# Performance work log

Hardware: AMD Instinct MI355X
Metric: run time of the kernel (lower is better)

Reference implementation:

```python
import jax, jax.numpy as jnp
import numpy as np

SEQ = 4096
E = 2048

def setup_inputs() -> dict:
    key = jax.random.key(0)
    kx, kq, kk, kv = jax.random.split(key, 4)
    scale = 1.0 / np.sqrt(E)
    x = jax.random.normal(kx, (SEQ, E), dtype=jnp.float32)
    # nn.Linear weights: shape [out, in], applied as x @ W.T
    Wq = jax.random.uniform(kq, (E, E), dtype=jnp.float32, minval=-scale, maxval=scale)
    Wk = jax.random.uniform(kk, (E, E), dtype=jnp.float32, minval=-scale, maxval=scale)
    Wv = jax.random.uniform(kv, (E, E), dtype=jnp.float32, minval=-scale, maxval=scale)
    return {"x": x, "Wq": Wq, "Wk": Wk, "Wv": Wv}

def reference(x, Wq, Wk, Wv):
    # q/k/v projections: nn.Linear(bias=False) -> x @ W.T
    q = x @ Wq.T  # [S, E]
    k = x @ Wk.T  # [S, E]
    v = x @ Wv.T  # [S, E]
    s = q @ k.T  # [S, S]
    w = jax.nn.softmax(s / jnp.sqrt(jnp.float32(E)), axis=-1)
    return w @ v  # [S, E]
```

## Files before the change

kernel.cpp:

```cpp
#include <hip/hip_runtime.h>
#include <hip/hip_bf16.h>

#define S_DIM 4096
#define E_DIM 2048

typedef __attribute__((ext_vector_type(4))) float f32x4;
typedef __attribute__((ext_vector_type(8))) short bf16x8;

__device__ __forceinline__ unsigned short f2bf(float f) {
  unsigned u = __builtin_bit_cast(unsigned, f);
  u += 0x7FFFu + ((u >> 16) & 1u);
  return (unsigned short)(u >> 16);
}
__device__ __forceinline__ float bf2f(unsigned short h) {
  return __builtin_bit_cast(float, ((unsigned)h) << 16);
}

__global__ __launch_bounds__(256) void cast_kernel(const float* __restrict__ in,
                                                   unsigned short* __restrict__ out,
                                                   int n4) {
  int i = blockIdx.x * 256 + threadIdx.x;
  if (i >= n4) return;
  float4 v = reinterpret_cast<const float4*>(in)[i];
  ushort4 o;
  o.x = f2bf(v.x); o.y = f2bf(v.y); o.z = f2bf(v.z); o.w = f2bf(v.w);
  reinterpret_cast<ushort4*>(out)[i] = o;
}


__device__ __forceinline__ void stage_tile(char* lds_tile, const unsigned short* g,
                                           int row0, int k0, int ld, int tid) {
#pragma unroll
  for (int p = 0; p < 2; ++p) {
    const int off = tid * 16 + p * 4096;
    const int row = off >> 6;
    const int colb = off & 63;
    const char* ga = reinterpret_cast<const char*>(g + (size_t)(row0 + row) * ld + k0) + colb;
    char* la = lds_tile + (off & ~1023);
    __builtin_amdgcn_global_load_lds(
        (const __attribute__((address_space(1))) void*)ga,
        (__attribute__((address_space(3))) void*)la,
        16, 0, 0);
  }
}

enum { EPI_TBF16 = 1, EPI_F32 = 2, EPI_BF16 = 3 };

template <int EPI>
__global__ __launch_bounds__(256, 2) void gemm_nt(
    const unsigned short* __restrict__ A, const unsigned short* __restrict__ B,
    int lda, int ldb, int K,
    float* __restrict__ Cf, unsigned short* __restrict__ Cb,
    int ldc, float scale) {
  extern __shared__ char smem[];
  char* sA = smem;
  char* sB = smem + 8192;

  const int tid = threadIdx.x;
  const int row0A = blockIdx.y * 128;
  const int row0B = blockIdx.x * 128;

  const int wave = tid >> 6;
  const int lane = tid & 63;
  const int wr = (wave >> 1) * 64;
  const int wc = (wave & 1) * 64;
  const int l15 = lane & 15;
  const int kg = lane >> 4;

  f32x4 acc[4][4];
#pragma unroll
  for (int m = 0; m < 4; ++m)
#pragma unroll
    for (int n = 0; n < 4; ++n) acc[m][n] = (f32x4){0.f, 0.f, 0.f, 0.f};

  for (int kt = 0; kt < K; kt += 32) {
    __syncthreads();
    stage_tile(sA, A, row0A, kt, lda, tid);
    stage_tile(sB, B, row0B, kt, ldb, tid);
    __syncthreads();

    bf16x8 a_f[4], b_f[4];
#pragma unroll
    for (int m = 0; m < 4; ++m) {
      const int ra = (wr + m * 16 + l15) * 64 + kg * 16;
      const int rb = (wc + m * 16 + l15) * 64 + kg * 16;
      a_f[m] = *reinterpret_cast<const bf16x8*>(sA + ra);
      b_f[m] = *reinterpret_cast<const bf16x8*>(sB + rb);
    }
#pragma unroll
    for (int m = 0; m < 4; ++m)
#pragma unroll
      for (int n = 0; n < 4; ++n)
        acc[m][n] = __builtin_amdgcn_mfma_f32_16x16x32_bf16(a_f[m], b_f[n], acc[m][n], 0, 0, 0);
  }

#pragma unroll
  for (int m = 0; m < 4; ++m)
#pragma unroll
    for (int n = 0; n < 4; ++n) {
      const int row = row0A + wr + m * 16 + kg * 4;
      const int col = row0B + wc + n * 16 + l15;
      f32x4 v = acc[m][n];
      if constexpr (EPI == EPI_F32) {
#pragma unroll
        for (int r = 0; r < 4; ++r)
          Cf[(size_t)(row + r) * ldc + col] = v[r] * scale;
      } else if constexpr (EPI == EPI_BF16) {
#pragma unroll
        for (int r = 0; r < 4; ++r)
          Cb[(size_t)(row + r) * ldc + col] = f2bf(v[r] * scale);
      } else {
        unsigned short tmp[4];
#pragma unroll
        for (int r = 0; r < 4; ++r) tmp[r] = f2bf(v[r] * scale);
        ushort4 pk;
        pk.x = tmp[0]; pk.y = tmp[1]; pk.z = tmp[2]; pk.w = tmp[3];
        *reinterpret_cast<ushort4*>(Cb + (size_t)col * ldc + row) = pk;
      }
    }
}

__global__ __launch_bounds__(256) void softmax_kernel(const unsigned short* __restrict__ Sm,
                                                      unsigned short* __restrict__ P) {
  const int row = blockIdx.x;
  const int tid = threadIdx.x;
  const unsigned short* src = Sm + (size_t)row * S_DIM;
  float vals[16];
  float mx = -1e30f;
#pragma unroll
  for (int i = 0; i < 4; ++i) {
    ushort4 h = reinterpret_cast<const ushort4*>(src)[tid + i * 256];
    float a = bf2f(h.x), b = bf2f(h.y), c = bf2f(h.z), d = bf2f(h.w);
    vals[i * 4 + 0] = a; vals[i * 4 + 1] = b;
    vals[i * 4 + 2] = c; vals[i * 4 + 3] = d;
    mx = fmaxf(mx, fmaxf(fmaxf(a, b), fmaxf(c, d)));
  }
#pragma unroll
  for (int off = 32; off >= 1; off >>= 1) mx = fmaxf(mx, __shfl_xor(mx, off, 64));
  __shared__ float red[8];
  const int wave = tid >> 6, lane = tid & 63;
  if (lane == 0) red[wave] = mx;
  __syncthreads();
  mx = fmaxf(fmaxf(red[0], red[1]), fmaxf(red[2], red[3]));
  float sum = 0.f;
#pragma unroll
  for (int i = 0; i < 16; ++i) { vals[i] = __expf(vals[i] - mx); sum += vals[i]; }
#pragma unroll
  for (int off = 32; off >= 1; off >>= 1) sum += __shfl_xor(sum, off, 64);
  if (lane == 0) red[4 + wave] = sum;
  __syncthreads();
  sum = red[4] + red[5] + red[6] + red[7];
  const float inv = 1.0f / sum;
  unsigned short* dst = P + (size_t)row * S_DIM;
#pragma unroll
  for (int i = 0; i < 4; ++i) {
    ushort4 pk;
    pk.x = f2bf(vals[i * 4 + 0] * inv);
    pk.y = f2bf(vals[i * 4 + 1] * inv);
    pk.z = f2bf(vals[i * 4 + 2] * inv);
    pk.w = f2bf(vals[i * 4 + 3] * inv);
    reinterpret_cast<ushort4*>(dst)[tid + i * 256] = pk;
  }
}

extern "C" void kernel_launch(void* const* d_in, const int* in_sizes, int n_in,
                              void* d_out, int out_size, void* d_ws, size_t ws_size,
                              hipStream_t stream) {
  const float* x  = (const float*)d_in[0];
  const float* Wq = (const float*)d_in[1];
  const float* Wk = (const float*)d_in[2];
  const float* Wv = (const float*)d_in[3];
  float* out = (float*)d_out;
  char* ws = (char*)d_ws;

  const size_t MB = 1024 * 1024;
  const size_t NEED = 104 * MB;
  if (ws_size < NEED) return;

  unsigned short* qb = (unsigned short*)(ws);
  unsigned short* kb = (unsigned short*)(ws + 16 * MB);
  unsigned short* vt = (unsigned short*)(ws + 32 * MB);
  unsigned short* xb = (unsigned short*)(ws + 48 * MB);
  unsigned short* wb = (unsigned short*)(ws + 64 * MB);
  unsigned short* Sb = (unsigned short*)(ws + 72 * MB);
  unsigned short* P  = qb;

  const int nx4 = S_DIM * E_DIM / 4;
  const int nw4 = E_DIM * E_DIM / 4;

  cast_kernel<<<(nx4 + 255) / 256, 256, 0, stream>>>(x, xb, nx4);

  dim3 gProj(E_DIM / 128, S_DIM / 128);
  cast_kernel<<<(nw4 + 255) / 256, 256, 0, stream>>>(Wq, wb, nw4);
  gemm_nt<EPI_BF16><<<gProj, 256, 16384, stream>>>(
      xb, wb, E_DIM, E_DIM, E_DIM, nullptr, qb, E_DIM, 1.0f);
  cast_kernel<<<(nw4 + 255) / 256, 256, 0, stream>>>(Wk, wb, nw4);
  gemm_nt<EPI_BF16><<<gProj, 256, 16384, stream>>>(
      xb, wb, E_DIM, E_DIM, E_DIM, nullptr, kb, E_DIM, 1.0f);
  cast_kernel<<<(nw4 + 255) / 256, 256, 0, stream>>>(Wv, wb, nw4);
  gemm_nt<EPI_TBF16><<<gProj, 256, 16384, stream>>>(
      xb, wb, E_DIM, E_DIM, E_DIM, nullptr, vt, S_DIM, 1.0f);

  dim3 gQK(S_DIM / 128, S_DIM / 128);
  const float scale = 0.022097086912079608f;
  gemm_nt<EPI_BF16><<<gQK, 256, 16384, stream>>>(
      qb, kb, E_DIM, E_DIM, E_DIM, nullptr, Sb, S_DIM, scale);

  softmax_kernel<<<S_DIM, 256, 0, stream>>>(Sb, P);

  dim3 gPV(E_DIM / 128, S_DIM / 128);
  gemm_nt<EPI_F32><<<gPV, 256, 16384, stream>>>(
      P, vt, S_DIM, S_DIM, S_DIM, out, nullptr, E_DIM, 1.0f);
}
```

Measured before the change: 445.6 us.

## Replace GEMMs with 256x256 double-buffered 8-wave kernel, fuse QKV, split-K PV

Replaces the 128x128 single-buffered GEMM with a 512-thread kernel using 256x256 tiles and a 64-wide K step. It double-buffers LDS with swizzled async global-to-LDS loads and interleaves MFMA phases with barriers and priority hints. The three projections are fused into one GEMM over concatenated weights, and the P@V GEMM uses split-K over two partial buffers followed by an add kernel. This aims to raise MFMA utilisation and data reuse, at the cost of 128KB LDS per block, more workspace, and an extra reduction pass.

```diff
diff --git a/kernel.cpp b/kernel.cpp
--- a/kernel.cpp
+++ b/kernel.cpp
@@ -27,97 +27,205 @@
   reinterpret_cast<ushort4*>(out)[i] = o;
 }
 
-
-__device__ __forceinline__ void stage_tile(char* lds_tile, const unsigned short* g,
-                                           int row0, int k0, int ld, int tid) {
+__global__ __launch_bounds__(256) void add_kernel(const float* __restrict__ a,
+                                                  const float* __restrict__ b,
+                                                  float* __restrict__ o, int n4) {
+  int i = blockIdx.x * 256 + threadIdx.x;
+  if (i >= n4) return;
+  float4 va = reinterpret_cast<const float4*>(a)[i];
+  float4 vb = reinterpret_cast<const float4*>(b)[i];
+  float4 vo = {va.x + vb.x, va.y + vb.y, va.z + vb.z, va.w + vb.w};
+  reinterpret_cast<float4*>(o)[i] = vo;
+}
+
+
+__device__ __forceinline__ void stage_half(const unsigned short* __restrict__ g,
+                                           int grow0, int ld, int kByte0,
+                                           char* ldsHalfBase, int tid) {
 #pragma unroll
   for (int p = 0; p < 2; ++p) {
-    const int off = tid * 16 + p * 4096;
-    const int row = off >> 6;
-    const int colb = off & 63;
-    const char* ga = reinterpret_cast<const char*>(g + (size_t)(row0 + row) * ld + k0) + colb;
-    char* la = lds_tile + (off & ~1023);
+    const int o = (p * 512 + tid) * 16;
+    const int S = o >> 10;
+    const int oi = o & 1023;
+    const int osi = oi ^ (((oi >> 9) & 1) << 5);
+    const int r  = (S >> 1) * 16 + (osi >> 6);
+    const int cb = (S & 1) * 64 + (osi & 63);
+    const char* ga = reinterpret_cast<const char*>(g) +
+                     ((size_t)(grow0 + r) * ld) * 2 + kByte0 + cb;
+    char* la = ldsHalfBase + (o & ~1023);
     __builtin_amdgcn_global_load_lds(
         (const __attribute__((address_space(1))) void*)ga,
-        (__attribute__((address_space(3))) void*)la,
-        16, 0, 0);
-  }
-}
-
-enum { EPI_TBF16 = 1, EPI_F32 = 2, EPI_BF16 = 3 };
+        (__attribute__((address_space(3))) void*)la, 16, 0, 0);
+  }
+}
+
+#define MFMA_QUAD(AM, AN, AF, BF)                                              \
+  _Pragma("unroll") for (int mm = 0; mm < 4; ++mm)                             \
+  _Pragma("unroll") for (int nn = 0; nn < 2; ++nn)                             \
+  _Pragma("unroll") for (int ks = 0; ks < 2; ++ks)                             \
+    acc[(AM) + mm][(AN) + nn] = __builtin_amdgcn_mfma_f32_16x16x32_bf16(       \
+        AF[mm][ks], BF[nn][ks], acc[(AM) + mm][(AN) + nn], 0, 0, 0);
+
+enum { EPI_QKV = 0, EPI_BF16 = 1, EPI_F32 = 2 };
 
 template <int EPI>
-__global__ __launch_bounds__(256, 2) void gemm_nt(
+__global__ __launch_bounds__(512, 2) void gemm8(
     const unsigned short* __restrict__ A, const unsigned short* __restrict__ B,
     int lda, int ldb, int K,
     float* __restrict__ Cf, unsigned short* __restrict__ Cb,
-    int ldc, float scale) {
-  extern __shared__ char smem[];
-  char* sA = smem;
-  char* sB = smem + 8192;
+    unsigned short* __restrict__ Ct, int ldc, float scale,
+    int kElemPerZ, long long zStrideC) {
+  extern __shared__ char lds[];
 
   const int tid = threadIdx.x;
-  const int row0A = blockIdx.y * 128;
-  const int row0B = blockIdx.x * 128;
+  const int rowA0 = blockIdx.y * 256;
+  const int rowB0 = blockIdx.x * 256;
+  const int k0B = blockIdx.z * kElemPerZ * 2;
+  if (EPI == EPI_F32) Cf += (size_t)blockIdx.z * zStrideC;
 
   const int wave = tid >> 6;
   const int lane = tid & 63;
-  const int wr = (wave >> 1) * 64;
-  const int wc = (wave & 1) * 64;
+  const int wm = wave >> 2;
+  const int wn = wave & 3;
   const int l15 = lane & 15;
   const int kg = lane >> 4;
-
-  f32x4 acc[4][4];
-#pragma unroll
-  for (int m = 0; m < 4; ++m)
-#pragma unroll
-    for (int n = 0; n < 4; ++n) acc[m][n] = (f32x4){0.f, 0.f, 0.f, 0.f};
-
-  for (int kt = 0; kt < K; kt += 32) {
-    __syncthreads();
-    stage_tile(sA, A, row0A, kt, lda, tid);
-    stage_tile(sB, B, row0B, kt, ldb, tid);
-    __syncthreads();
-
-    bf16x8 a_f[4], b_f[4];
-#pragma unroll
-    for (int m = 0; m < 4; ++m) {
-      const int ra = (wr + m * 16 + l15) * 64 + kg * 16;
-      const int rb = (wc + m * 16 + l15) * 64 + kg * 16;
-      a_f[m] = *reinterpret_cast<const bf16x8*>(sA + ra);
-      b_f[m] = *reinterpret_cast<const bf16x8*>(sB + rb);
+  const int rsw = (l15 * 64 + kg * 16) ^ ((l15 & 8) << 2);
+
+  int bSub[2][2];
+#pragma unroll
+  for (int nh = 0; nh < 2; ++nh)
+#pragma unroll
+    for (int nn = 0; nn < 2; ++nn) {
+      const int row = wn * 64 + nh * 32 + nn * 16;
+      bSub[nh][nn] = 32768 + (row >> 7) * 16384 + ((row & 127) >> 4) * 2048;
     }
-#pragma unroll
-    for (int m = 0; m < 4; ++m)
-#pragma unroll
-      for (int n = 0; n < 4; ++n)
-        acc[m][n] = __builtin_amdgcn_mfma_f32_16x16x32_bf16(a_f[m], b_f[n], acc[m][n], 0, 0, 0);
-  }
-
-#pragma unroll
-  for (int m = 0; m < 4; ++m)
-#pragma unroll
-    for (int n = 0; n < 4; ++n) {
-      const int row = row0A + wr + m * 16 + kg * 4;
-      const int col = row0B + wc + n * 16 + l15;
-      f32x4 v = acc[m][n];
+  const int aBase = wm * 16384;
+
+  f32x4 acc[8][4];
+#pragma unroll
+  for (int mi = 0; mi < 8; ++mi)
+#pragma unroll
+    for (int ni = 0; ni < 4; ++ni) acc[mi][ni] = (f32x4){0.f, 0.f, 0.f, 0.f};
+
+  const int NT = K / 64;
+  char* buf0 = lds;
+  char* buf1 = lds + 65536;
+
+  stage_half(A, rowA0,       lda, k0B,       buf0 + 0,     tid);
+  stage_half(A, rowA0 + 128, lda, k0B,       buf0 + 16384, tid);
+  stage_half(B, rowB0,       ldb, k0B,       buf0 + 32768, tid);
+  stage_half(B, rowB0 + 128, ldb, k0B,       buf0 + 49152, tid);
+  stage_half(A, rowA0,       lda, k0B + 128, buf1 + 0,     tid);
+  stage_half(A, rowA0 + 128, lda, k0B + 128, buf1 + 16384, tid);
+  stage_half(B, rowB0,       ldb, k0B + 128, buf1 + 32768, tid);
+  asm volatile("s_waitcnt vmcnt(6)" ::: "memory");
+  __builtin_amdgcn_sched_barrier(0);
+  __builtin_amdgcn_s_barrier();
+
+  for (int t = 0; t < NT; ++t) {
+    char* bufc = lds + (t & 1) * 65536;
+    char* bufn = lds + ((t & 1) ^ 1) * 65536;
+    bf16x8 a0[4][2], a1[4][2], b0[2][2], b1[2][2];
+
+#pragma unroll
+    for (int mm = 0; mm < 4; ++mm)
+#pragma unroll
+      for (int ks = 0; ks < 2; ++ks)
+        a0[mm][ks] = *reinterpret_cast<const bf16x8*>(
+            bufc + aBase + (mm * 2 + ks) * 1024 + rsw);
+#pragma unroll
+    for (int nn = 0; nn < 2; ++nn)
+#pragma unroll
+      for (int ks = 0; ks < 2; ++ks)
+        b0[nn][ks] = *reinterpret_cast<const bf16x8*>(
+            bufc + bSub[0][nn] + ks * 1024 + rsw);
+    if (t + 1 < NT)
+      stage_half(B, rowB0 + 128, ldb, k0B + (t + 1) * 128, bufn + 49152, tid);
+    asm volatile("s_waitcnt lgkmcnt(8)" ::: "memory");
+    __builtin_amdgcn_s_barrier();
+    asm volatile("s_waitcnt lgkmcnt(0)" ::: "memory");
+    __builtin_amdgcn_sched_barrier(0);
+    __builtin_amdgcn_s_setprio(1);
+    MFMA_QUAD(0, 0, a0, b0)
+    __builtin_amdgcn_s_setprio(0);
+    __builtin_amdgcn_s_barrier();
+
+#pragma unroll
+    for (int nn = 0; nn < 2; ++nn)
+#pragma unroll
+      for (int ks = 0; ks < 2; ++ks)
+        b1[nn][ks] = *reinterpret_cast<const bf16x8*>(
+            bufc + bSub[1][nn] + ks * 1024 + rsw);
+    __builtin_amdgcn_s_barrier();
+    asm volatile("s_waitcnt lgkmcnt(0)" ::: "memory");
+    __builtin_amdgcn_sched_barrier(0);
+    __builtin_amdgcn_s_setprio(1);
+    MFMA_QUAD(0, 2, a0, b1)
+    __builtin_amdgcn_s_setprio(0);
+    __builtin_amdgcn_s_barrier();
+
+#pragma unroll
+    for (int mm = 0; mm < 4; ++mm)
+#pragma unroll
+      for (int ks = 0; ks < 2; ++ks)
+        a1[mm][ks] = *reinterpret_cast<const bf16x8*>(
+            bufc + aBase + ((4 + mm) * 2 + ks) * 1024 + rsw);
+    __builtin_amdgcn_s_barrier();
+    asm volatile("s_waitcnt lgkmcnt(0)" ::: "memory");
+    __builtin_amdgcn_sched_barrier(0);
+    __builtin_amdgcn_s_setprio(1);
+    MFMA_QUAD(4, 2, a1, b1)
+    __builtin_amdgcn_s_setprio(0);
+    __builtin_amdgcn_s_barrier();
+
+    if (t + 2 < NT) {
+      const int kb = k0B + (t + 2) * 128;
+      stage_half(A, rowA0,       lda, kb, bufc + 0,     tid);
+      stage_half(A, rowA0 + 128, lda, kb, bufc + 16384, tid);
+      stage_half(B, rowB0,       ldb, kb, bufc + 32768, tid);
+      asm volatile("s_waitcnt vmcnt(6)" ::: "memory");
+    } else {
+      asm volatile("s_waitcnt vmcnt(0)" ::: "memory");
+    }
+    __builtin_amdgcn_sched_barrier(0);
+    __builtin_amdgcn_s_barrier();
+    __builtin_amdgcn_s_setprio(1);
+    MFMA_QUAD(4, 0, a1, b0)
+    __builtin_amdgcn_s_setprio(0);
+    __builtin_amdgcn_s_barrier();
+  }
+
+  const int r0 = rowA0 + wm * 128;
+  const int c0 = rowB0 + wn * 64;
+#pragma unroll
+  for (int mi = 0; mi < 8; ++mi) {
+    const int row = r0 + (mi >> 2) * 64 + (mi & 3) * 16 + kg * 4;
+#pragma unroll
+    for (int ni = 0; ni < 4; ++ni) {
+      const int col = c0 + (ni >> 1) * 32 + (ni & 1) * 16 + l15;
+      f32x4 v = acc[mi][ni];
       if constexpr (EPI == EPI_F32) {
 #pragma unroll
         for (int r = 0; r < 4; ++r)
-          Cf[(size_t)(row + r) * ldc + col] = v[r] * scale;
+          Cf[(size_t)(row + r) * ldc + col] = v[r];
       } else if constexpr (EPI == EPI_BF16) {
 #pragma unroll
         for (int r = 0; r < 4; ++r)
           Cb[(size_t)(row + r) * ldc + col] = f2bf(v[r] * scale);
       } else {
-        unsigned short tmp[4];
-#pragma unroll
-        for (int r = 0; r < 4; ++r) tmp[r] = f2bf(v[r] * scale);
-        ushort4 pk;
-        pk.x = tmp[0]; pk.y = tmp[1]; pk.z = tmp[2]; pk.w = tmp[3];
-        *reinterpret_cast<ushort4*>(Cb + (size_t)col * ldc + row) = pk;
+        if (rowB0 < 4096) {
+#pragma unroll
+          for (int r = 0; r < 4; ++r)
+            Cb[(size_t)(row + r) * 4096 + col] = f2bf(v[r]);
+        } else {
+          ushort4 pk;
+          pk.x = f2bf(v[0]); pk.y = f2bf(v[1]);
+          pk.z = f2bf(v[2]); pk.w = f2bf(v[3]);
+          *reinterpret_cast<ushort4*>(Ct + (size_t)(col - 4096) * 4096 + row) = pk;
+        }
       }
     }
+  }
 }
 
 __global__ __launch_bounds__(256) void softmax_kernel(const unsigned short* __restrict__ Sm,
@@ -174,41 +282,45 @@
   char* ws = (char*)d_ws;
 
   const size_t MB = 1024 * 1024;
-  const size_t NEED = 104 * MB;
+  const size_t NEED = 120 * MB;
   if (ws_size < NEED) return;
 
-  unsigned short* qb = (unsigned short*)(ws);
-  unsigned short* kb = (unsigned short*)(ws + 16 * MB);
-  unsigned short* vt = (unsigned short*)(ws + 32 * MB);
-  unsigned short* xb = (unsigned short*)(ws + 48 * MB);
-  unsigned short* wb = (unsigned short*)(ws + 64 * MB);
-  unsigned short* Sb = (unsigned short*)(ws + 72 * MB);
-  unsigned short* P  = qb;
+  unsigned short* xb   = (unsigned short*)(ws);
+  unsigned short* wcat = (unsigned short*)(ws + 16 * MB);
+  unsigned short* qkb  = (unsigned short*)(ws + 40 * MB);
+  unsigned short* vt   = (unsigned short*)(ws + 72 * MB);
+  unsigned short* Sb   = (unsigned short*)(ws + 88 * MB);
+  float* outp0 = (float*)(ws);
+  float* outp1 = (float*)(ws + 88 * MB);
+  unsigned short* P = qkb;
+
+  hipFuncSetAttribute(reinterpret_cast<const void*>(&gemm8<EPI_QKV>),
+                      hipFuncAttributeMaxDynamicSharedMemorySize, 131072);
+  hipFuncSetAttribute(reinterpret_cast<const void*>(&gemm8<EPI_BF16>),
+                      hipFuncAttributeMaxDynamicSharedMemorySize, 131072);
+  hipFuncSetAttribute(reinterpret_cast<const void*>(&gemm8<EPI_F32>),
+                      hipFuncAttributeMaxDynamicSharedMemorySize, 131072);
 
   const int nx4 = S_DIM * E_DIM / 4;
   const int nw4 = E_DIM * E_DIM / 4;
 
-  cast_kernel<<<(nx4 + 255) / 256, 256, 0, stream>>>(x, xb, nx4);
-
-  dim3 gProj(E_DIM / 128, S_DIM / 128);
-  cast_kernel<<<(nw4 + 255) / 256, 256, 0, stream>>>(Wq, wb, nw4);
-  gemm_nt<EPI_BF16><<<gProj, 256, 16384, stream>>>(
-      xb, wb, E_DIM, E_DIM, E_DIM, nullptr, qb, E_DIM, 1.0f);
-  cast_kernel<<<(nw4 + 255) / 256, 256, 0, stream>>>(Wk, wb, nw4);
-  gemm_nt<EPI_BF16><<<gProj, 256, 16384, stream>>>(
-      xb, wb, E_DIM, E_DIM, E_DIM, nullptr, kb, E_DIM, 1.0f);
-  cast_kernel<<<(nw4 + 255) / 256, 256, 0, stream>>>(Wv, wb, nw4);
-  gemm_nt<EPI_TBF16><<<gProj, 256, 16384, stream>>>(
-      xb, wb, E_DIM, E_DIM, E_DIM, nullptr, vt, S_DIM, 1.0f);
-
-  dim3 gQK(S_DIM / 128, S_DIM / 128);
+  cast_kernel<<<nx4 / 256, 256, 0, stream>>>(x, xb, nx4);
+  cast_kernel<<<nw4 / 256, 256, 0, stream>>>(Wq, wcat, nw4);
+  cast_kernel<<<nw4 / 256, 256, 0, stream>>>(Wk, wcat + (size_t)2048 * 2048, nw4);
+  cast_kernel<<<nw4 / 256, 256, 0, stream>>>(Wv, wcat + (size_t)4096 * 2048, nw4);
+
+  gemm8<EPI_QKV><<<dim3(24, 16, 1), 512, 131072, stream>>>(
+      xb, wcat, E_DIM, E_DIM, E_DIM, nullptr, qkb, vt, 4096, 1.0f, 0, 0);
+
   const float scale = 0.022097086912079608f;
-  gemm_nt<EPI_BF16><<<gQK, 256, 16384, stream>>>(
-      qb, kb, E_DIM, E_DIM, E_DIM, nullptr, Sb, S_DIM, scale);
+  gemm8<EPI_BF16><<<dim3(16, 16, 1), 512, 131072, stream>>>(
+      qkb, qkb + 2048, 4096, 4096, E_DIM, nullptr, Sb, nullptr, 4096, scale, 0, 0);
 
   softmax_kernel<<<S_DIM, 256, 0, stream>>>(Sb, P);
 
-  dim3 gPV(E_DIM / 128, S_DIM / 128);
-  gemm_nt<EPI_F32><<<gPV, 256, 16384, stream>>>(
-      P, vt, S_DIM, S_DIM, S_DIM, out, nullptr, E_DIM, 1.0f);
-}
+  gemm8<EPI_F32><<<dim3(8, 16, 2), 512, 131072, stream>>>(
+      P, vt, 4096, 4096, 2048, outp0, nullptr, nullptr, E_DIM, 1.0f,
+      2048, (long long)(88 * MB) / 4);
+
+  add_kernel<<<nx4 / 256, 256, 0, stream>>>(outp0, outp1, out, nx4);
+}
```

New measurement: 418.4 us. -6.1%, faster.
